# Kernel tuning notes

Measured on AMD Instinct MI355X. Metric: run time of the kernel, lower is better.

## Reference

```python
import jax, jax.numpy as jnp
import numpy as np

B, N, D, H, E, W, OUT = 4, 2048, 128, 4, 32768, 8, 128


def setup_inputs() -> dict:
    key = jax.random.key(0)
    ks = jax.random.split(key, 11)
    s = 0.05  # weight init scale
    return {
        "nodefeatures": jax.random.normal(ks[0], (B, N, D), jnp.float32),
        "node_indices": jax.random.randint(ks[1], (B, 2, E), 0, N),
        "nodeattributes": jax.random.uniform(ks[2], (B, E, W), jnp.float32),
        "wq_w": jax.random.normal(ks[3], (H, D, D), jnp.float32) * s,
        "wq_b": jax.random.normal(ks[4], (H, D), jnp.float32) * s,
        "wk_w": jax.random.normal(ks[5], (H, D, D), jnp.float32) * s,
        "wk_b": jax.random.normal(ks[6], (H, D), jnp.float32) * s,
        "wv_w": jax.random.normal(ks[7], (H, D, D), jnp.float32) * s,
        "wv_b": jax.random.normal(ks[8], (H, D), jnp.float32) * s,
        "out_w": jax.random.normal(ks[9], (OUT, H * D), jnp.float32) * s,
        "out_b": jax.random.normal(ks[10], (OUT,), jnp.float32) * s,
    }


def reference(nodefeatures, node_indices, nodeattributes,
              wq_w, wq_b, wk_w, wk_b, wv_w, wv_b, out_w, out_b):
    b, n, d = nodefeatures.shape
    h = wq_w.shape[0]
    # per-head Linear projections: y = x @ W.T + bias, batched over heads -> [b,h,n,d]
    q = jnp.einsum('bnd,hed->bhne', nodefeatures, wq_w) + wq_b[None, :, None, :]
    k = jnp.einsum('bnd,hed->bhne', nodefeatures, wk_w) + wk_b[None, :, None, :]
    v = jnp.einsum('bnd,hed->bhne', nodefeatures, wv_w) + wv_b[None, :, None, :]

    i = node_indices[:, 0, :]  # [b,E] row indices
    j = node_indices[:, 1, :]  # [b,E] col indices

    # gather q_i, k_j per edge -> [b,h,E,d]; edge score = <q_i,k_j>/sqrt(n)
    qi = jnp.take_along_axis(q, i[:, None, :, None], axis=2)
    kj = jnp.take_along_axis(k, j[:, None, :, None], axis=2)
    wsum = nodeattributes.sum(axis=-1)  # [b,E] (x_edge[:,None]*weights).sum(1)
    # original divides by k.shape[1]**0.5 == sqrt(n)
    edge = (qi * kj).sum(-1) / (n ** 0.5) * wsum[:, None, :]  # [b,h,E]

    # scatter edge scores into zero-initialized dense logits [b,h,n,n]
    bi = jnp.arange(b)[:, None, None]
    hi = jnp.arange(h)[None, :, None]
    scores = jnp.zeros((b, h, n, n), q.dtype).at[bi, hi, i[:, None, :], j[:, None, :]].set(edge)

    attn = jax.nn.softmax(scores, axis=-1)
    o = jnp.einsum('bhnm,bhmd->bhnd', attn, v)
    o = o.transpose(0, 2, 1, 3).reshape(b, n, h * d)  # concat heads on feature dim
    return o @ out_w.T + out_b
```

## Files before the change

### kernel.cpp

```cpp
#include <hip/hip_runtime.h>
#include <hip/hip_bf16.h>
#include <math.h>

constexpr int B_ = 4;
constexpr int N_ = 2048;
constexpr int D_ = 128;
constexpr int H_ = 4;
constexpr int E_ = 32768;
constexpr int W_ = 8;
constexpr int OUT_ = 128;
constexpr int HD_ = H_ * D_;
constexpr int C3_ = 3 * HD_;
constexpr int CAP = 64;
constexpr int M_ = B_ * N_;

typedef __attribute__((ext_vector_type(8))) __bf16 bf16x8;
typedef __attribute__((ext_vector_type(4))) float f32x4;
typedef unsigned int uint32;
typedef unsigned short u16;

__device__ __forceinline__ u16 f2b(float f) {
    __hip_bfloat16 h = __float2bfloat16(f);
    return *(u16*)&h;
}
__device__ __forceinline__ float blo(uint32 u) { return __uint_as_float(u << 16); }
__device__ __forceinline__ float bhi(uint32 u) { return __uint_as_float(u & 0xffff0000u); }

__device__ __forceinline__ void g2l16(const void* g, void* l) {
    __builtin_amdgcn_global_load_lds(
        (const __attribute__((address_space(1))) unsigned int*)(uintptr_t)g,
        (__attribute__((address_space(3))) unsigned int*)(uintptr_t)l,
        16, 0, 0);
}

__global__ __launch_bounds__(256) void prep_kernel(
    const float* __restrict__ X,
    const float* __restrict__ wq, const float* __restrict__ wk, const float* __restrict__ wv,
    const float* __restrict__ bq, const float* __restrict__ bk, const float* __restrict__ bv,
    const float* __restrict__ OW,
    u16* __restrict__ Xbf, u16* __restrict__ Wbf, float* __restrict__ biasf,
    u16* __restrict__ OWbf,
    int* __restrict__ row_count, float* __restrict__ vsum)
{
    const int blk = blockIdx.x;
    if (blk < 512) {
        const int tid = blk * 256 + threadIdx.x;
        const float4 f0 = *(const float4*)(X + (size_t)tid * 8);
        const float4 f1 = *(const float4*)(X + (size_t)tid * 8 + 4);
        union { u16 u[8]; uint4 v; } pk;
        pk.u[0]=f2b(f0.x); pk.u[1]=f2b(f0.y); pk.u[2]=f2b(f0.z); pk.u[3]=f2b(f0.w);
        pk.u[4]=f2b(f1.x); pk.u[5]=f2b(f1.y); pk.u[6]=f2b(f1.z); pk.u[7]=f2b(f1.w);
        *(uint4*)((char*)Xbf + (size_t)tid * 16) = pk.v;
    } else if (blk < 608) {
        const int c = (blk - 512) * 256 + threadIdx.x;
        const int g = c >> 11, idx = c & 2047;
        const int t3 = g >> 2, h = g & 3;
        const float* Wsrc = (t3 == 0 ? wq : t3 == 1 ? wk : wv) + (size_t)h * 128 * 128;
        const float4 f0 = *(const float4*)(Wsrc + (size_t)idx * 8);
        const float4 f1 = *(const float4*)(Wsrc + (size_t)idx * 8 + 4);
        union { u16 u[8]; uint4 v; } pk;
        pk.u[0]=f2b(f0.x); pk.u[1]=f2b(f0.y); pk.u[2]=f2b(f0.z); pk.u[3]=f2b(f0.w);
        pk.u[4]=f2b(f1.x); pk.u[5]=f2b(f1.y); pk.u[6]=f2b(f1.z); pk.u[7]=f2b(f1.w);
        *(uint4*)((char*)Wbf + (size_t)c * 16) = pk.v;
        if (idx < 128) {
            const float* Bsrc = (t3 == 0 ? bq : t3 == 1 ? bk : bv) + h * 128;
            biasf[g * 128 + idx] = Bsrc[idx];
        }
    } else if (blk < 640) {
        const int tid = (blk - 608) * 256 + threadIdx.x;
        const int c = tid >> 6, sub = tid & 63;
        const float4 f0 = *(const float4*)(OW + (size_t)c * 512 + sub * 8);
        const float4 f1 = *(const float4*)(OW + (size_t)c * 512 + sub * 8 + 4);
        union { u16 u[8]; uint4 v; } pk;
        pk.u[0]=f2b(f0.x); pk.u[1]=f2b(f0.y); pk.u[2]=f2b(f0.z); pk.u[3]=f2b(f0.w);
        pk.u[4]=f2b(f1.x); pk.u[5]=f2b(f1.y); pk.u[6]=f2b(f1.z); pk.u[7]=f2b(f1.w);
        const int ob = c * 1024 + ((sub * 16) ^ ((c & 7) << 4));
        *(uint4*)((char*)OWbf + ob) = pk.v;
    } else {
        const uint4 z = make_uint4(0, 0, 0, 0);
        uint4* rc = (uint4*)row_count;
        #pragma unroll
        for (int q = 0; q < 8; ++q) rc[threadIdx.x + q * 256] = z;
        uint4* vs = (uint4*)vsum;
        #pragma unroll
        for (int q = 0; q < 2; ++q) vs[threadIdx.x + q * 256] = z;
    }
}

__global__ __launch_bounds__(256) void qkv_append(
    const u16* __restrict__ Xbf, const u16* __restrict__ Wbf,
    const float* __restrict__ biasf,
    const int* __restrict__ nidx, const float* __restrict__ attr,
    u16* __restrict__ QKV, float* __restrict__ vsum,
    int* __restrict__ row_count, int2* __restrict__ row_edges)
{
    __shared__ u16 Cs[128 * 128];
    const int t = threadIdx.x;
    const int lane = t & 63, wave = t >> 6;

    if (blockIdx.x >= 768) {
        const int gw = (blockIdx.x - 768) * 4 + wave;
        const int e0g = gw * 8;
        const int b = e0g / E_;
        const int e0 = e0g % E_;
        float a = attr[((size_t)b * E_ + e0) * W_ + lane];
        a += __shfl_xor(a, 1);
        a += __shfl_xor(a, 2);
        a += __shfl_xor(a, 4);
        if ((lane & 7) == 0) {
            const int sub = lane >> 3;
            const int e = e0 + sub;
            const int i = nidx[b * 2 * E_ + e];
            const int j = nidx[b * 2 * E_ + E_ + e];
            const int pos = atomicAdd(&row_count[b * N_ + i], 1);
            if (pos < CAP)
                row_edges[(size_t)(b * N_ + i) * CAP + pos] =
                    make_int2(e | (j << 16), __float_as_int(a));
        }
        return;
    }

    const int rb = blockIdx.x & 63;
    const int g  = blockIdx.x >> 6;
    const int wm = wave >> 1, wn = wave & 1;
    const int l15 = lane & 15, l4 = lane >> 4;

    const u16* Abase = Xbf + (size_t)(rb * 128) * 128;
    const u16* Bbase = Wbf + (size_t)(g  * 128) * 128;

    f32x4 acc[4][4];
    #pragma unroll
    for (int i = 0; i < 4; ++i)
        #pragma unroll
        for (int j = 0; j < 4; ++j) acc[i][j] = (f32x4){0.f, 0.f, 0.f, 0.f};

    #pragma unroll
    for (int ks = 0; ks < 4; ++ks) {
        const int ko = ks * 32 + l4 * 8;
        bf16x8 a[4], bb[4];
        #pragma unroll
        for (int fm = 0; fm < 4; ++fm)
            a[fm] = *(const bf16x8*)(Abase + (wm * 64 + fm * 16 + l15) * 128 + ko);
        #pragma unroll
        for (int fn = 0; fn < 4; ++fn)
            bb[fn] = *(const bf16x8*)(Bbase + (wn * 64 + fn * 16 + l15) * 128 + ko);
        #pragma unroll
        for (int fm = 0; fm < 4; ++fm)
            #pragma unroll
            for (int fn = 0; fn < 4; ++fn)
                acc[fm][fn] = __builtin_amdgcn_mfma_f32_16x16x32_bf16(
                    a[fm], bb[fn], acc[fm][fn], 0, 0, 0);
    }

    #pragma unroll
    for (int fm = 0; fm < 4; ++fm)
        #pragma unroll
        for (int fn = 0; fn < 4; ++fn) {
            const int col = wn * 64 + fn * 16 + l15;
            const float bv = biasf[g * 128 + col];
            #pragma unroll
            for (int r = 0; r < 4; ++r) {
                const int row = wm * 64 + fm * 16 + l4 * 4 + r;
                *(u16*)((char*)Cs + row * 256 + ((col * 2) ^ ((row & 7) << 4))) =
                    f2b(acc[fm][fn][r] + bv);
            }
        }

    if (g >= 8) {
        const int h = g - 8;
        const int b = rb >> 4;
        #pragma unroll
        for (int fn = 0; fn < 4; ++fn) {
            float s = 0.f;
            #pragma unroll
            for (int fm = 0; fm < 4; ++fm)
                #pragma unroll
                for (int r = 0; r < 4; ++r) s += acc[fm][fn][r];
            s += __shfl_xor(s, 16);
            s += __shfl_xor(s, 32);
            if (l4 == 0) {
                const int col = wn * 64 + fn * 16 + l15;
                const float bv = biasf[g * 128 + col];
                atomicAdd(&vsum[(b * H_ + h) * 128 + col], s + 64.f * bv);
            }
        }
    }
    __syncthreads();

    #pragma unroll
    for (int q = 0; q < 8; ++q) {
        const int idx = t + q * 256;
        const int row = idx >> 4, c = idx & 15;
        const uint4 v = *(const uint4*)((char*)Cs + row * 256 + ((c * 16) ^ ((row & 7) << 4)));
        *(uint4*)(QKV + (size_t)(rb * 128 + row) * C3_ + g * 128 + c * 8) = v;
    }
}

__global__ __launch_bounds__(256) void row_fused(
    const u16* __restrict__ QKV, const float* __restrict__ vsum,
    const int* __restrict__ row_count, const int2* __restrict__ row_edges,
    u16* __restrict__ Obf)
{
    const int t = threadIdx.x;
    const int wave = t >> 6, lane = t & 63;
    const int gid = blockIdx.x;
    const int xcd = gid & 7;
    const int b = xcd >> 1;
    const int rowgrp = ((xcd & 1) << 8) | (gid >> 3);
    const int row = rowgrp * 4 + wave;
    const int R = b * N_ + row;
    int cnt = row_count[R];
    if (cnt > CAP) cnt = CAP;

    int ej = 0; float ws = 0.f;
    if (lane < cnt) {
        const int2 v = row_edges[(size_t)R * CAP + lane];
        ej = v.x; ws = __int_as_float(v.y);
    }
    const int myj = ej >> 16, mye = ej & 0xFFFF;
    bool win = (lane < cnt);
    for (int p = 0; p < cnt; ++p) {
        const int oj = __shfl(ej, p);
        if (win && (oj >> 16) == myj && (oj & 0xFFFF) > mye) win = false;
    }
    unsigned long long m = __ballot(win);

    const char* base = (const char*)QKV;
    const uint4 qv = *(const uint4*)(base + (size_t)R * 3072 + lane * 16);
    const float q0=blo(qv.x), q1=bhi(qv.x), q2=blo(qv.y), q3=bhi(qv.y),
                q4=blo(qv.z), q5=bhi(qv.z), q6=blo(qv.w), q7=bhi(qv.w);
    const float rs = 0.02209708691207961f;

    float A0=0.f,A1=0.f,A2=0.f,A3=0.f,A4=0.f,A5=0.f,A6=0.f,A7=0.f;
    float B0=0.f,B1=0.f,B2=0.f,B3=0.f,B4=0.f,B5=0.f,B6=0.f,B7=0.f;
    float dsA = 0.f, dsB = 0.f;

#define FETCH(MM, KV1,VV1,W1,KV2,VV2,W2,NN)                                  \
    { int p_ = (int)__ffsll((long long)MM) - 1; MM &= MM - 1;                \
      const int j_ = __shfl(ej, p_) >> 16; W1 = __shfl(ws, p_);              \
      const char* nb_ = base + (size_t)(b * N_ + j_) * 3072;                 \
      KV1 = *(const uint4*)(nb_ + 1024 + lane * 16);                         \
      VV1 = *(const uint4*)(nb_ + 2048 + lane * 16);                         \
      if (MM) {                                                              \
        int q_ = (int)__ffsll((long long)MM) - 1; MM &= MM - 1;              \
        const int j2_ = __shfl(ej, q_) >> 16; W2 = __shfl(ws, q_);           \
        const char* nb2_ = base + (size_t)(b * N_ + j2_) * 3072;             \
        KV2 = *(const uint4*)(nb2_ + 1024 + lane * 16);                      \
        VV2 = *(const uint4*)(nb2_ + 2048 + lane * 16);                      \
        NN = 2;                                                              \
      } else NN = 1; }

#define PROC(kv, vv, wsp, S)                                                 \
    { float s_ = q0*blo(kv.x) + q1*bhi(kv.x) + q2*blo(kv.y) + q3*bhi(kv.y)   \
               + q4*blo(kv.z) + q5*bhi(kv.z) + q6*blo(kv.w) + q7*bhi(kv.w);  \
      s_ += __shfl_xor(s_, 1);                                               \
      s_ += __shfl_xor(s_, 2);                                               \
      s_ += __shfl_xor(s_, 4);                                               \
      s_ += __shfl_xor(s_, 8);                                               \
      const float x_ = expf(s_ * rs * (wsp)) - 1.f;                          \
      ds##S += x_;                                                           \
      S##0 = fmaf(x_, blo(vv.x), S##0); S##1 = fmaf(x_, bhi(vv.x), S##1);    \
      S##2 = fmaf(x_, blo(vv.y), S##2); S##3 = fmaf(x_, bhi(vv.y), S##3);    \
      S##4 = fmaf(x_, blo(vv.z), S##4); S##5 = fmaf(x_, bhi(vv.z), S##5);    \
      S##6 = fmaf(x_, blo(vv.w), S##6); S##7 = fmaf(x_, bhi(vv.w), S##7); }

    if (m) {
        uint4 kv1, vv1, kv2, vv2; float w1, w2; int n1;
        FETCH(m, kv1, vv1, w1, kv2, vv2, w2, n1);
        while (m) {
            uint4 nk1, nv1, nk2, nv2; float nw1, nw2; int n2;
            FETCH(m, nk1, nv1, nw1, nk2, nv2, nw2, n2);
            PROC(kv1, vv1, w1, A);
            if (n1 == 2) PROC(kv2, vv2, w2, B);
            kv1 = nk1; vv1 = nv1; w1 = nw1;
            kv2 = nk2; vv2 = nv2; w2 = nw2; n1 = n2;
        }
        PROC(kv1, vv1, w1, A);
        if (n1 == 2) PROC(kv2, vv2, w2, B);
    }
#undef FETCH
#undef PROC

    const float inv = 1.0f / (2048.0f + dsA + dsB);
    const float* vsp = vsum + (b * H_ + (lane >> 4)) * 128 + (lane & 15) * 8;
    const float4 vs0 = *(const float4*)vsp;
    const float4 vs1 = *(const float4*)(vsp + 4);
    union { u16 u[8]; uint4 v; } o;
    o.u[0]=f2b((vs0.x+A0+B0)*inv); o.u[1]=f2b((vs0.y+A1+B1)*inv);
    o.u[2]=f2b((vs0.z+A2+B2)*inv); o.u[3]=f2b((vs0.w+A3+B3)*inv);
    o.u[4]=f2b((vs1.x+A4+B4)*inv); o.u[5]=f2b((vs1.y+A5+B5)*inv);
    o.u[6]=f2b((vs1.z+A6+B6)*inv); o.u[7]=f2b((vs1.w+A7+B7)*inv);
    const int ob = ((lane >> 4) << 8) + (((lane & 15) * 16) ^ ((R & 7) << 4));
    *(uint4*)((char*)Obf + (size_t)R * 1024 + ob) = o.v;
}

__global__ __launch_bounds__(256) void out_mfma(
    const u16* __restrict__ Obf, const u16* __restrict__ OWbf,
    const float* __restrict__ bo, float* __restrict__ Out)
{
    __shared__ u16 As[32 * 128];
    __shared__ u16 Bs[128 * 128];
    const int rb = blockIdx.x;
    const int t = threadIdx.x;
    const int lane = t & 63, wave = t >> 6;
    const int wm = wave >> 1, wn = wave & 1;
    const int l15 = lane & 15, l4 = lane >> 4;

    f32x4 acc[4];
    #pragma unroll
    for (int j = 0; j < 4; ++j) acc[j] = (f32x4){0.f, 0.f, 0.f, 0.f};

    for (int kc = 0; kc < 4; ++kc) {
        #pragma unroll
        for (int q = 0; q < 2; ++q) {
            const int o = t * 16 + q * 4096;
            const int arow = o >> 8, ob = o & 255;
            g2l16((const char*)Obf + (size_t)(rb * 32 + arow) * 1024 + kc * 256 + ob,
                  (char*)As + o);
        }
        #pragma unroll
        for (int q = 0; q < 8; ++q) {
            const int o = t * 16 + q * 4096;
            const int c = o >> 8, ob = o & 255;
            g2l16((const char*)OWbf + (size_t)c * 1024 + kc * 256 + ob,
                  (char*)Bs + o);
        }
        __syncthreads();
        #pragma unroll
        for (int ks = 0; ks < 4; ++ks) {
            const int kb = ks * 64 + l4 * 16;
            bf16x8 a0, bb[4];
            {
                const int row = wm * 16 + l15;
                a0 = *(const bf16x8*)((const char*)As + row * 256 + (kb ^ ((row & 7) << 4)));
            }
            #pragma unroll
            for (int fn = 0; fn < 4; ++fn) {
                const int col = wn * 64 + fn * 16 + l15;
                bb[fn] = *(const bf16x8*)((const char*)Bs + col * 256 + (kb ^ ((col & 7) << 4)));
            }
            #pragma unroll
            for (int fn = 0; fn < 4; ++fn)
                acc[fn] = __builtin_amdgcn_mfma_f32_16x16x32_bf16(
                    a0, bb[fn], acc[fn], 0, 0, 0);
        }
        __syncthreads();
    }

    #pragma unroll
    for (int fn = 0; fn < 4; ++fn) {
        const int col = wn * 64 + fn * 16 + l15;
        const float bv = bo[col];
        #pragma unroll
        for (int r = 0; r < 4; ++r) {
            const int row = rb * 32 + wm * 16 + l4 * 4 + r;
            Out[(size_t)row * OUT_ + col] = acc[fn][r] + bv;
        }
    }
}

extern "C" void kernel_launch(void* const* d_in, const int* in_sizes, int n_in,
                              void* d_out, int out_size, void* d_ws, size_t ws_size,
                              hipStream_t stream)
{
    const float* x     = (const float*)d_in[0];
    const int*   nidx  = (const int*)  d_in[1];
    const float* attr  = (const float*)d_in[2];
    const float* wq_w  = (const float*)d_in[3];
    const float* wq_b  = (const float*)d_in[4];
    const float* wk_w  = (const float*)d_in[5];
    const float* wk_b  = (const float*)d_in[6];
    const float* wv_w  = (const float*)d_in[7];
    const float* wv_b  = (const float*)d_in[8];
    const float* out_w = (const float*)d_in[9];
    const float* out_b = (const float*)d_in[10];
    float* out = (float*)d_out;

    char* ws = (char*)d_ws;
    size_t off = 0;
    auto alloc = [&](size_t bytes) -> char* {
        char* p = ws + off;
        off += (bytes + 255) & ~(size_t)255;
        return p;
    };
    u16*  Xbf  = (u16*)alloc((size_t)M_ * D_ * 2);
    u16*  Wbf  = (u16*)alloc((size_t)12 * D_ * D_ * 2);
    float* biasf = (float*)alloc((size_t)12 * D_ * 4);
    u16*  QKV  = (u16*)alloc((size_t)M_ * C3_ * 2);
    u16*  OWbf = (u16*)alloc((size_t)OUT_ * HD_ * 2);
    u16*  Obf  = (u16*)alloc((size_t)M_ * HD_ * 2);
    float* vsum = (float*)alloc((size_t)B_ * H_ * D_ * 4);
    int*  row_count = (int*)alloc((size_t)B_ * N_ * 4);
    int2* row_edges = (int2*)alloc((size_t)B_ * N_ * CAP * 8);

    prep_kernel<<<641, 256, 0, stream>>>(
        x, wq_w, wk_w, wv_w, wq_b, wk_b, wv_b, out_w,
        Xbf, Wbf, biasf, OWbf, row_count, vsum);
    qkv_append<<<768 + 4096, 256, 0, stream>>>(
        Xbf, Wbf, biasf, nidx, attr, QKV, vsum, row_count, row_edges);
    row_fused<<<2048, 256, 0, stream>>>(
        QKV, vsum, row_count, row_edges, Obf);
    out_mfma<<<M_ / 32, 256, 0, stream>>>(Obf, OWbf, out_b, out);
}
```

Before: 77.87 us.

## Move edge-append into prep kernel and zero counters with memset

```diff
diff --git a/kernel.cpp b/kernel.cpp
--- a/kernel.cpp
+++ b/kernel.cpp
@@ -33,18 +33,20 @@
         16, 0, 0);
 }
 
-__global__ __launch_bounds__(256) void prep_kernel(
+__global__ __launch_bounds__(256) void prep_append(
     const float* __restrict__ X,
     const float* __restrict__ wq, const float* __restrict__ wk, const float* __restrict__ wv,
     const float* __restrict__ bq, const float* __restrict__ bk, const float* __restrict__ bv,
     const float* __restrict__ OW,
+    const int* __restrict__ nidx, const float* __restrict__ attr,
     u16* __restrict__ Xbf, u16* __restrict__ Wbf, float* __restrict__ biasf,
     u16* __restrict__ OWbf,
-    int* __restrict__ row_count, float* __restrict__ vsum)
+    int* __restrict__ row_count, int2* __restrict__ row_edges)
 {
     const int blk = blockIdx.x;
+    const int t = threadIdx.x;
     if (blk < 512) {
-        const int tid = blk * 256 + threadIdx.x;
+        const int tid = blk * 256 + t;
         const float4 f0 = *(const float4*)(X + (size_t)tid * 8);
         const float4 f1 = *(const float4*)(X + (size_t)tid * 8 + 4);
         union { u16 u[8]; uint4 v; } pk;
@@ -52,7 +54,7 @@
         pk.u[4]=f2b(f1.x); pk.u[5]=f2b(f1.y); pk.u[6]=f2b(f1.z); pk.u[7]=f2b(f1.w);
         *(uint4*)((char*)Xbf + (size_t)tid * 16) = pk.v;
     } else if (blk < 608) {
-        const int c = (blk - 512) * 256 + threadIdx.x;
+        const int c = (blk - 512) * 256 + t;
         const int g = c >> 11, idx = c & 2047;
         const int t3 = g >> 2, h = g & 3;
         const float* Wsrc = (t3 == 0 ? wq : t3 == 1 ? wk : wv) + (size_t)h * 128 * 128;
@@ -67,7 +69,7 @@
             biasf[g * 128 + idx] = Bsrc[idx];
         }
     } else if (blk < 640) {
-        const int tid = (blk - 608) * 256 + threadIdx.x;
+        const int tid = (blk - 608) * 256 + t;
         const int c = tid >> 6, sub = tid & 63;
         const float4 f0 = *(const float4*)(OW + (size_t)c * 512 + sub * 8);
         const float4 f1 = *(const float4*)(OW + (size_t)c * 512 + sub * 8 + 4);
@@ -77,29 +79,8 @@
         const int ob = c * 1024 + ((sub * 16) ^ ((c & 7) << 4));
         *(uint4*)((char*)OWbf + ob) = pk.v;
     } else {
-        const uint4 z = make_uint4(0, 0, 0, 0);
-        uint4* rc = (uint4*)row_count;
-        #pragma unroll
-        for (int q = 0; q < 8; ++q) rc[threadIdx.x + q * 256] = z;
-        uint4* vs = (uint4*)vsum;
-        #pragma unroll
-        for (int q = 0; q < 2; ++q) vs[threadIdx.x + q * 256] = z;
-    }
-}
-
-__global__ __launch_bounds__(256) void qkv_append(
-    const u16* __restrict__ Xbf, const u16* __restrict__ Wbf,
-    const float* __restrict__ biasf,
-    const int* __restrict__ nidx, const float* __restrict__ attr,
-    u16* __restrict__ QKV, float* __restrict__ vsum,
-    int* __restrict__ row_count, int2* __restrict__ row_edges)
-{
-    __shared__ u16 Cs[128 * 128];
-    const int t = threadIdx.x;
-    const int lane = t & 63, wave = t >> 6;
-
-    if (blockIdx.x >= 768) {
-        const int gw = (blockIdx.x - 768) * 4 + wave;
+        const int wave = t >> 6, lane = t & 63;
+        const int gw = (blk - 640) * 4 + wave;
         const int e0g = gw * 8;
         const int b = e0g / E_;
         const int e0 = e0g % E_;
@@ -117,9 +98,17 @@
                 row_edges[(size_t)(b * N_ + i) * CAP + pos] =
                     make_int2(e | (j << 16), __float_as_int(a));
         }
-        return;
-    }
-
+    }
+}
+
+__global__ __launch_bounds__(256) void qkv_gemm(
+    const u16* __restrict__ Xbf, const u16* __restrict__ Wbf,
+    const float* __restrict__ biasf, u16* __restrict__ QKV,
+    float* __restrict__ vsum)
+{
+    __shared__ u16 Cs[128 * 128];
+    const int t = threadIdx.x;
+    const int lane = t & 63, wave = t >> 6;
     const int rb = blockIdx.x & 63;
     const int g  = blockIdx.x >> 6;
     const int wm = wave >> 1, wn = wave & 1;
@@ -383,21 +372,22 @@
         off += (bytes + 255) & ~(size_t)255;
         return p;
     };
+    u16*  QKV  = (u16*)alloc((size_t)M_ * C3_ * 2);
     u16*  Xbf  = (u16*)alloc((size_t)M_ * D_ * 2);
     u16*  Wbf  = (u16*)alloc((size_t)12 * D_ * D_ * 2);
     float* biasf = (float*)alloc((size_t)12 * D_ * 4);
-    u16*  QKV  = (u16*)alloc((size_t)M_ * C3_ * 2);
     u16*  OWbf = (u16*)alloc((size_t)OUT_ * HD_ * 2);
     u16*  Obf  = (u16*)alloc((size_t)M_ * HD_ * 2);
     float* vsum = (float*)alloc((size_t)B_ * H_ * D_ * 4);
     int*  row_count = (int*)alloc((size_t)B_ * N_ * 4);
     int2* row_edges = (int2*)alloc((size_t)B_ * N_ * CAP * 8);
 
-    prep_kernel<<<641, 256, 0, stream>>>(
-        x, wq_w, wk_w, wv_w, wq_b, wk_b, wv_b, out_w,
-        Xbf, Wbf, biasf, OWbf, row_count, vsum);
-    qkv_append<<<768 + 4096, 256, 0, stream>>>(
-        Xbf, Wbf, biasf, nidx, attr, QKV, vsum, row_count, row_edges);
+    hipMemsetAsync(vsum, 0, (size_t)B_ * H_ * D_ * 4 + (size_t)B_ * N_ * 4, stream);
+
+    prep_append<<<640 + 4096, 256, 0, stream>>>(
+        x, wq_w, wk_w, wv_w, wq_b, wk_b, wv_b, out_w, nidx, attr,
+        Xbf, Wbf, biasf, OWbf, row_count, row_edges);
+    qkv_gemm<<<768, 256, 0, stream>>>(Xbf, Wbf, biasf, QKV, vsum);
     row_fused<<<2048, 256, 0, stream>>>(
         QKV, vsum, row_count, row_edges, Obf);
     out_mfma<<<M_ / 32, 256, 0, stream>>>(Obf, OWbf, out_b, out);
```

Result: slower. 81.05 us (+4.1%).
